# Kernel optimization log

Hardware: AMD Instinct MI355X
Metric: run time of the kernel (lower is better)

Reference implementation:

```python
import jax, jax.numpy as jnp
import numpy as np

N_NODES = 50000
NEG_SLOPE = 0.2  # PyG GATConv default
EPS = 1e-16      # PyG softmax denominator epsilon


def gat_conv(x, W, att_src, att_dst, bias, src, dst, heads, out_ch):
    # x: [N, F_in]; W: [F_in, heads*out_ch]; att_*: [heads, out_ch]
    N = x.shape[0]
    h = (x @ W).reshape(N, heads, out_ch)              # [N,H,C]
    a_src = jnp.sum(h * att_src, axis=-1)              # [N,H]
    a_dst = jnp.sum(h * att_dst, axis=-1)              # [N,H]
    alpha = a_src[src] + a_dst[dst]                    # [E,H]
    alpha = jnp.where(alpha > 0, alpha, NEG_SLOPE * alpha)  # leaky_relu
    amax = jax.ops.segment_max(alpha, dst, num_segments=N)  # [N,H]
    amax = jnp.where(jnp.isfinite(amax), amax, 0.0)
    ex = jnp.exp(alpha - amax[dst])                    # [E,H]
    denom = jax.ops.segment_sum(ex, dst, num_segments=N)    # [N,H]
    coef = ex / (denom[dst] + EPS)                     # [E,H]
    msg = h[src] * coef[:, :, None]                    # [E,H,C]
    out = jax.ops.segment_sum(msg, dst, num_segments=N)     # [N,H,C]
    return out.reshape(N, heads * out_ch) + bias


def setup_inputs() -> dict:
    key = jax.random.key(0)
    ks = jax.random.split(key, 11)
    T, N, F = 8, N_NODES, 64
    E = 1_600_000
    x = jax.random.normal(ks[0], (T, N, F), dtype=jnp.float32)
    edge_index = jax.random.randint(ks[1], (2, E), 0, N, dtype=jnp.int64)
    s = 0.1
    return {
        "x": x,
        "edge_index": edge_index,
        "W1": jax.random.normal(ks[2], (F, 64), jnp.float32) * s,
        "att_src1": jax.random.normal(ks[3], (8, 8), jnp.float32) * s,
        "att_dst1": jax.random.normal(ks[4], (8, 8), jnp.float32) * s,
        "bias1": jax.random.normal(ks[5], (64,), jnp.float32) * s,
        "W2": jax.random.normal(ks[6], (64, F), jnp.float32) * s,
        "att_src2": jax.random.normal(ks[7], (1, F), jnp.float32) * s,
        "att_dst2": jax.random.normal(ks[8], (1, F), jnp.float32) * s,
        "bias2": jax.random.normal(ks[9], (F,), jnp.float32) * s,
    }


def reference(x, edge_index, W1, att_src1, att_dst1, bias1, W2, att_src2, att_dst2, bias2):
    N = x.shape[1]
    # PyG GATConv adds self-loops by default
    loops = jnp.arange(N, dtype=edge_index.dtype)
    src = jnp.concatenate([edge_index[0], loops])
    dst = jnp.concatenate([edge_index[1], loops])

    def step(xt):  # xt: [N, F] ; dropout is identity in eval mode
        y = jax.nn.elu(gat_conv(xt, W1, att_src1, att_dst1, bias1, src, dst, 8, 8))
        y = gat_conv(y, W2, att_src2, att_dst2, bias2, src, dst, 1, xt.shape[-1])
        return jax.nn.log_softmax(y, axis=-1)

    return jax.vmap(step)(x)  # [T, N, F]
```

## Files before the change

kernel.cpp:

```cpp
#include <hip/hip_runtime.h>
#include <hip/hip_bf16.h>
#include <math.h>


typedef __hip_bfloat16 bf16;

__device__ __forceinline__ float bf2f(unsigned short u) {
    return __uint_as_float(((unsigned int)u) << 16);
}


__global__ __launch_bounds__(256) void count_edges_kernel(const int* __restrict__ dsts,
                                                          int* cnt, int E) {
    int i = blockIdx.x * 256 + threadIdx.x;
    if (i < E) atomicAdd(&cnt[dsts[i]], 1);
}

__global__ __launch_bounds__(1024) void scan_kernel(const int* __restrict__ cnt,
                                                    int* row, int* cur, int N) {
    __shared__ int ls[1024];
    int t = threadIdx.x;
    int chunk = (N + 1023) / 1024;
    int b = t * chunk;
    int sum = 0;
    for (int i = 0; i < chunk; ++i) {
        int idx = b + i;
        if (idx < N) sum += cnt[idx] + 1;
    }
    ls[t] = sum;
    __syncthreads();
    for (int off = 1; off < 1024; off <<= 1) {
        int v = (t >= off) ? ls[t - off] : 0;
        __syncthreads();
        ls[t] += v;
        __syncthreads();
    }
    int run = (t == 0) ? 0 : ls[t - 1];
    for (int i = 0; i < chunk; ++i) {
        int idx = b + i;
        if (idx < N) {
            int c = cnt[idx] + 1;
            row[idx] = run;
            cur[idx] = run;
            run += c;
        }
    }
    if (t == 1023) row[N] = ls[1023];
}

__device__ __forceinline__ void fill_csr_body(int i, const int* __restrict__ srcs,
                                              const int* __restrict__ dsts,
                                              int* cur, int* esrc, int E, int N) {
    if (i >= E + N) return;
    int s, d;
    if (i < E) { s = srcs[i]; d = dsts[i]; }
    else       { s = i - E;   d = s; }
    int pos = atomicAdd(&cur[d], 1);
    esrc[pos] = s;
}

__global__ __launch_bounds__(256) void fill_csr_kernel(const int* __restrict__ srcs,
                                                       const int* __restrict__ dsts,
                                                       int* cur, int* esrc, int E, int N) {
    fill_csr_body(blockIdx.x * 256 + threadIdx.x, srcs, dsts, cur, esrc, E, N);
}


__device__ __forceinline__ float4 ld4(const float* p) { return *(const float4*)p; }
__device__ __forceinline__ float4 ld4(const bf16* p) {
    ushort4 u = *(const ushort4*)p;
    float4 r;
    r.x = bf2f(u.x); r.y = bf2f(u.y); r.z = bf2f(u.z); r.w = bf2f(u.w);
    return r;
}


template <typename TIN, int H, int C>
__device__ __forceinline__ void gemm_att_body(
    int bid,
    const TIN* __restrict__ xin,
    const float* __restrict__ Wm,
    const float* __restrict__ att_s,
    const float* __restrict__ att_d,
    bf16* __restrict__ hout,
    float* __restrict__ asrc,
    float* __restrict__ adst,
    int R) {
    __shared__ float Ws[64 * 64];
    int tid = threadIdx.x;
    {
        const float4* W4 = (const float4*)Wm;
        float4* Ws4 = (float4*)Ws;
#pragma unroll
        for (int i = 0; i < 4; ++i) Ws4[tid + 256 * i] = W4[tid + 256 * i];
    }
    __syncthreads();

    int c  = tid & 63;
    int wv = tid >> 6;
    int n0 = (bid * 4 + wv) * 4;
    if (n0 >= R) return;
    int nrows = (R - n0 >= 4) ? 4 : (R - n0);

    const TIN* xb = xin + (size_t)n0 * 64;
    float acc[4] = {0.f, 0.f, 0.f, 0.f};

#pragma unroll 2
    for (int k4 = 0; k4 < 16; ++k4) {
        float4 xv[4];
#pragma unroll
        for (int r = 0; r < 4; ++r) {
            int rr = (r < nrows) ? r : 0;
            xv[r] = ld4(xb + (size_t)rr * 64 + k4 * 4);
        }
        float w0 = Ws[(4 * k4 + 0) * 64 + c];
        float w1 = Ws[(4 * k4 + 1) * 64 + c];
        float w2 = Ws[(4 * k4 + 2) * 64 + c];
        float w3 = Ws[(4 * k4 + 3) * 64 + c];
#pragma unroll
        for (int r = 0; r < 4; ++r) {
            acc[r] = fmaf(xv[r].x, w0, acc[r]);
            acc[r] = fmaf(xv[r].y, w1, acc[r]);
            acc[r] = fmaf(xv[r].z, w2, acc[r]);
            acc[r] = fmaf(xv[r].w, w3, acc[r]);
        }
    }

    float as_w = att_s[c];
    float ad_w = att_d[c];
#pragma unroll
    for (int r = 0; r < 4; ++r) {
        if (r >= nrows) break;
        int n = n0 + r;
        float a = acc[r];
        hout[(size_t)n * 64 + c] = __float2bfloat16(a);
        float vs = a * as_w;
        float vd = a * ad_w;
#pragma unroll
        for (int off = 1; off < C; off <<= 1) {
            vs += __shfl_xor(vs, off, 64);
            vd += __shfl_xor(vd, off, 64);
        }
        if ((c % C) == 0) {
            int hd = c / C;
            asrc[(size_t)n * H + hd] = vs;
            adst[(size_t)n * H + hd] = vd;
        }
    }
}

template <typename TIN, int H, int C>
__global__ __launch_bounds__(256) void gemm_att_kernel(
    const TIN* __restrict__ xin, const float* __restrict__ Wm,
    const float* __restrict__ att_s, const float* __restrict__ att_d,
    bf16* __restrict__ hout, float* __restrict__ asrc, float* __restrict__ adst, int R) {
    gemm_att_body<TIN, H, C>(blockIdx.x, xin, Wm, att_s, att_d, hout, asrc, adst, R);
}

template <typename TIN, int H, int C>
__global__ __launch_bounds__(256) void gemm_fill_kernel(
    const TIN* __restrict__ xin, const float* __restrict__ Wm,
    const float* __restrict__ att_s, const float* __restrict__ att_d,
    bf16* __restrict__ hout, float* __restrict__ asrc, float* __restrict__ adst, int R,
    const int* __restrict__ srcs, const int* __restrict__ dsts,
    int* cur, int* esrc, int E, int N, int fill_blocks) {
    if ((int)blockIdx.x < fill_blocks) {
        fill_csr_body((int)blockIdx.x * 256 + threadIdx.x, srcs, dsts, cur, esrc, E, N);
    } else {
        gemm_att_body<TIN, H, C>((int)blockIdx.x - fill_blocks,
                                 xin, Wm, att_s, att_d, hout, asrc, adst, R);
    }
}


template <int H, bool FINAL>
__global__ __launch_bounds__(256) void gat_edge_kernel(
    const bf16* __restrict__ h_all,
    const float* __restrict__ asrc_all,
    const float* __restrict__ adst_all,
    const int* __restrict__ row,
    const int* __restrict__ esrc,
    const float* __restrict__ bias,
    bf16* __restrict__ outb,
    float* __restrict__ outf,
    int N, int BPT) {
    int tid  = threadIdx.x;
    int lane = tid & 63;
    int t  = blockIdx.x / BPT;
    int nb = blockIdx.x - t * BPT;
    int n  = nb * 4 + (tid >> 6);
    if (n >= N) return;

    const bf16*  h     = h_all    + (size_t)t * N * 64;
    const char*  asrcb = (const char*)(asrc_all + (size_t)t * N * H);
    const float* adst  = adst_all + (size_t)t * N * H;

    const int head = (H == 8) ? (lane >> 3) : 0;
    float adn = adst[(size_t)n * H + head];

    int e0  = row[n];
    int deg = row[n + 1] - e0;

    float lsum_lane = 0.f;
    float acc0 = 0.f, acc1 = 0.f;

    for (int base = 0; base < deg; base += 64) {
        int cnt = deg - base; if (cnt > 64) cnt = 64;
        int sv = (lane < cnt) ? esrc[e0 + base + lane] : 0;

        if constexpr (H == 8) {
            unsigned head4 = (unsigned)(head << 2);
            unsigned l7_4  = (unsigned)((lane & 7) << 2);
#pragma unroll
            for (int sub = 0; sub < 8; ++sub) {
                if (sub * 8 >= cnt) break;
                int svj = __builtin_amdgcn_ds_bpermute((sub * 32) + l7_4, sv);
                unsigned aoff = (((unsigned)svj) << 5) | head4;
                float av = *(const float*)(asrcb + aoff);
                float tv = av + adn;
                tv = tv > 0.f ? tv : 0.2f * tv;
                tv = (sub * 8 + (lane & 7) < cnt) ? tv : -INFINITY;
                float p = __expf(tv);
                lsum_lane += p;
                unsigned pu = __float_as_uint(p);
#define ACC_EDGE(Q)                                                            \
    {                                                                          \
        float pj = __uint_as_float(                                            \
            __builtin_amdgcn_ds_swizzle(pu, ((Q) << 5) | 0x18));               \
        unsigned sj = (unsigned)__builtin_amdgcn_readlane(sv, sub * 8 + (Q));  \
        const unsigned short* hrow =                                           \
            (const unsigned short*)h + ((size_t)sj << 6);    \
        float hvf = bf2f(hrow[lane]);                                          \
        if ((Q) & 1) acc1 = fmaf(pj, hvf, acc1);                               \
        else         acc0 = fmaf(pj, hvf, acc0);                               \
    }
                ACC_EDGE(0) ACC_EDGE(1) ACC_EDGE(2) ACC_EDGE(3)
                ACC_EDGE(4) ACC_EDGE(5) ACC_EDGE(6) ACC_EDGE(7)
#undef ACC_EDGE
            }
        } else {
            unsigned aoff = ((unsigned)sv) << 2;
            float av = *(const float*)(asrcb + aoff);
            float tv = av + adn;
            tv = tv > 0.f ? tv : 0.2f * tv;
            tv = (lane < cnt) ? tv : -INFINITY;
            float p0 = __expf(tv);
            lsum_lane += p0;
            for (int j0 = 0; j0 < cnt; j0 += 8) {
#pragma unroll
                for (int q = 0; q < 8; ++q) {
                    int j = j0 + q;
                    float pj = __uint_as_float(
                        __builtin_amdgcn_readlane(__float_as_uint(p0), j));
                    unsigned sj = (unsigned)__builtin_amdgcn_readlane(sv, j);
                    const unsigned short* hrow =
                        (const unsigned short*)h + ((size_t)sj << 6);
                    float hvf = bf2f(hrow[lane]);
                    if (q & 1) acc1 = fmaf(pj, hvf, acc1);
                    else       acc0 = fmaf(pj, hvf, acc0);
                }
            }
        }
    }

    float lsum;
    if constexpr (H == 8) {
        float ls = lsum_lane;
        ls += __shfl_xor(ls, 1, 64);
        ls += __shfl_xor(ls, 2, 64);
        ls += __shfl_xor(ls, 4, 64);
        lsum = ls;
    } else {
        float ls = lsum_lane;
#pragma unroll
        for (int o = 1; o < 64; o <<= 1) ls += __shfl_xor(ls, o, 64);
        lsum = ls;
    }

    float v = (acc0 + acc1) / (lsum + 1e-16f) + bias[lane];
    size_t oidx = ((size_t)t * N + n) * 64 + lane;
    if (!FINAL) {
        float y = v > 0.f ? v : expm1f(v);
        outb[oidx] = __float2bfloat16(y);
    } else {
        float mx = v;
#pragma unroll
        for (int off = 1; off < 64; off <<= 1) mx = fmaxf(mx, __shfl_xor(mx, off, 64));
        float ex = __expf(v - mx);
        float sm = ex;
#pragma unroll
        for (int off = 1; off < 64; off <<= 1) sm += __shfl_xor(sm, off, 64);
        outf[oidx] = (v - mx) - __logf(sm);
    }
}


extern "C" void kernel_launch(void* const* d_in, const int* in_sizes, int n_in,
                              void* d_out, int out_size, void* d_ws, size_t ws_size,
                              hipStream_t stream) {
    const float* x        = (const float*)d_in[0];
    const int*   eidx     = (const int*)d_in[1];
    const float* W1       = (const float*)d_in[2];
    const float* att_src1 = (const float*)d_in[3];
    const float* att_dst1 = (const float*)d_in[4];
    const float* bias1    = (const float*)d_in[5];
    const float* W2       = (const float*)d_in[6];
    const float* att_src2 = (const float*)d_in[7];
    const float* att_dst2 = (const float*)d_in[8];
    const float* bias2    = (const float*)d_in[9];
    float* dout = (float*)d_out;

    const int N = 50000;
    const int F = 64;
    const int E = in_sizes[1] / 2;
    const int T = in_sizes[0] / (N * F);
    const int NT = T * N;
    const int Etot = E + N;
    const int BPT = (N + 3) / 4;

    const int* srcs = eidx;
    const int* dsts = eidx + E;

    char* ws = (char*)d_ws;
    size_t off = 0;
    auto carve = [&](size_t bytes) -> void* {
        void* p = ws + off;
        off = (off + bytes + 255) & ~(size_t)255;
        return p;
    };
    bf16*  h_all  = (bf16*)carve((size_t)NT * 64 * sizeof(bf16));
    bf16*  y1_all = (bf16*)carve((size_t)NT * 64 * sizeof(bf16));
    float* asrc   = (float*)carve((size_t)NT * 8 * sizeof(float));
    float* adst   = (float*)carve((size_t)NT * 8 * sizeof(float));
    int*   rowp   = (int*)carve((size_t)(N + 1) * sizeof(int));
    int*   cnt    = (int*)carve((size_t)N * sizeof(int));
    int*   cur    = (int*)carve((size_t)N * sizeof(int));
    int*   esrc   = (int*)carve((size_t)Etot * sizeof(int));
    bool batched = (off <= ws_size);

    if (batched) {
        hipMemsetAsync(cnt, 0, (size_t)N * sizeof(int), stream);
        count_edges_kernel<<<(E + 255) / 256, 256, 0, stream>>>(dsts, cnt, E);
        scan_kernel<<<1, 1024, 0, stream>>>(cnt, rowp, cur, N);

        int gemm_blocks = (NT + 15) / 16;
        int fill_blocks = (E + N + 255) / 256;
        int edge_grid = BPT * T;
        gemm_fill_kernel<float, 8, 8><<<fill_blocks + gemm_blocks, 256, 0, stream>>>(
            x, W1, att_src1, att_dst1, h_all, asrc, adst, NT,
            srcs, dsts, cur, esrc, E, N, fill_blocks);
        gat_edge_kernel<8, false><<<edge_grid, 256, 0, stream>>>(
            h_all, asrc, adst, rowp, esrc, bias1, y1_all, nullptr, N, BPT);
        gemm_att_kernel<bf16, 1, 64><<<gemm_blocks, 256, 0, stream>>>(
            y1_all, W2, att_src2, att_dst2, h_all, asrc, adst, NT);
        gat_edge_kernel<1, true><<<edge_grid, 256, 0, stream>>>(
            h_all, asrc, adst, rowp, esrc, bias2, nullptr, dout, N, BPT);
    } else {
        off = 0;
        bf16*  h1  = (bf16*)carve((size_t)N * 64 * sizeof(bf16));
        bf16*  y1  = (bf16*)carve((size_t)N * 64 * sizeof(bf16));
        float* as1 = (float*)carve((size_t)N * 8 * sizeof(float));
        float* ad1 = (float*)carve((size_t)N * 8 * sizeof(float));
        int*   rp  = (int*)carve((size_t)(N + 1) * sizeof(int));
        int*   cn  = (int*)carve((size_t)N * sizeof(int));
        int*   cu  = (int*)carve((size_t)N * sizeof(int));
        int*   es  = (int*)carve((size_t)Etot * sizeof(int));
        hipMemsetAsync(cn, 0, (size_t)N * sizeof(int), stream);
        count_edges_kernel<<<(E + 255) / 256, 256, 0, stream>>>(dsts, cn, E);
        scan_kernel<<<1, 1024, 0, stream>>>(cn, rp, cu, N);
        fill_csr_kernel<<<(E + N + 255) / 256, 256, 0, stream>>>(srcs, dsts, cu, es, E, N);
        int gemm_grid = (N + 15) / 16;
        for (int t = 0; t < T; ++t) {
            const float* xt = x + (size_t)t * N * F;
            float* ot = dout + (size_t)t * N * F;
            gemm_att_kernel<float, 8, 8><<<gemm_grid, 256, 0, stream>>>(
                xt, W1, att_src1, att_dst1, h1, as1, ad1, N);
            gat_edge_kernel<8, false><<<(N + 3) / 4, 256, 0, stream>>>(
                h1, as1, ad1, rp, es, bias1, y1, nullptr, N, (N + 3) / 4);
            gemm_att_kernel<bf16, 1, 64><<<gemm_grid, 256, 0, stream>>>(
                y1, W2, att_src2, att_dst2, h1, as1, ad1, N);
            gat_edge_kernel<1, true><<<(N + 3) / 4, 256, 0, stream>>>(
                h1, as1, ad1, rp, es, bias2, nullptr, ot, N, (N + 3) / 4);
        }
    }
}
```

Measured before the change: 1.164 ms.

## Batch attention gathers in edge kernel and split fused CSR-fill/GEMM launch

In the 8-head edge kernel, all eight attention-score gathers for a 64-edge chunk are now issued before any exp or accumulation, so the gather latencies overlap instead of being serialized per 8-edge sub-group. The feature gather loop then runs in 16-edge steps, and the single-head path's unroll goes from 8 to 16 to keep more loads in flight. The fused fill-CSR plus GEMM launch is split back into two separate kernels. That removes the fused launch's chance to overlap the atomic-heavy CSR fill with the GEMM, and the extra unrolling raises register pressure.

```diff
diff --git a/kernel.cpp b/kernel.cpp
--- a/kernel.cpp
+++ b/kernel.cpp
@@ -48,9 +48,10 @@
     if (t == 1023) row[N] = ls[1023];
 }
 
-__device__ __forceinline__ void fill_csr_body(int i, const int* __restrict__ srcs,
-                                              const int* __restrict__ dsts,
-                                              int* cur, int* esrc, int E, int N) {
+__global__ __launch_bounds__(256) void fill_csr_kernel(const int* __restrict__ srcs,
+                                                       const int* __restrict__ dsts,
+                                                       int* cur, int* esrc, int E, int N) {
+    int i = blockIdx.x * 256 + threadIdx.x;
     if (i >= E + N) return;
     int s, d;
     if (i < E) { s = srcs[i]; d = dsts[i]; }
@@ -59,12 +60,6 @@
     esrc[pos] = s;
 }
 
-__global__ __launch_bounds__(256) void fill_csr_kernel(const int* __restrict__ srcs,
-                                                       const int* __restrict__ dsts,
-                                                       int* cur, int* esrc, int E, int N) {
-    fill_csr_body(blockIdx.x * 256 + threadIdx.x, srcs, dsts, cur, esrc, E, N);
-}
-
 
 __device__ __forceinline__ float4 ld4(const float* p) { return *(const float4*)p; }
 __device__ __forceinline__ float4 ld4(const bf16* p) {
@@ -76,8 +71,7 @@
 
 
 template <typename TIN, int H, int C>
-__device__ __forceinline__ void gemm_att_body(
-    int bid,
+__global__ __launch_bounds__(256) void gemm_att_kernel(
     const TIN* __restrict__ xin,
     const float* __restrict__ Wm,
     const float* __restrict__ att_s,
@@ -98,7 +92,7 @@
 
     int c  = tid & 63;
     int wv = tid >> 6;
-    int n0 = (bid * 4 + wv) * 4;
+    int n0 = (blockIdx.x * 4 + wv) * 4;
     if (n0 >= R) return;
     int nrows = (R - n0 >= 4) ? 4 : (R - n0);
 
@@ -146,29 +140,6 @@
             asrc[(size_t)n * H + hd] = vs;
             adst[(size_t)n * H + hd] = vd;
         }
-    }
-}
-
-template <typename TIN, int H, int C>
-__global__ __launch_bounds__(256) void gemm_att_kernel(
-    const TIN* __restrict__ xin, const float* __restrict__ Wm,
-    const float* __restrict__ att_s, const float* __restrict__ att_d,
-    bf16* __restrict__ hout, float* __restrict__ asrc, float* __restrict__ adst, int R) {
-    gemm_att_body<TIN, H, C>(blockIdx.x, xin, Wm, att_s, att_d, hout, asrc, adst, R);
-}
-
-template <typename TIN, int H, int C>
-__global__ __launch_bounds__(256) void gemm_fill_kernel(
-    const TIN* __restrict__ xin, const float* __restrict__ Wm,
-    const float* __restrict__ att_s, const float* __restrict__ att_d,
-    bf16* __restrict__ hout, float* __restrict__ asrc, float* __restrict__ adst, int R,
-    const int* __restrict__ srcs, const int* __restrict__ dsts,
-    int* cur, int* esrc, int E, int N, int fill_blocks) {
-    if ((int)blockIdx.x < fill_blocks) {
-        fill_csr_body((int)blockIdx.x * 256 + threadIdx.x, srcs, dsts, cur, esrc, E, N);
-    } else {
-        gemm_att_body<TIN, H, C>((int)blockIdx.x - fill_blocks,
-                                 xin, Wm, att_s, att_d, hout, asrc, adst, R);
     }
 }
 
@@ -211,33 +182,47 @@
         if constexpr (H == 8) {
             unsigned head4 = (unsigned)(head << 2);
             unsigned l7_4  = (unsigned)((lane & 7) << 2);
+            float av[8];
 #pragma unroll
             for (int sub = 0; sub < 8; ++sub) {
-                if (sub * 8 >= cnt) break;
-                int svj = __builtin_amdgcn_ds_bpermute((sub * 32) + l7_4, sv);
-                unsigned aoff = (((unsigned)svj) << 5) | head4;
-                float av = *(const float*)(asrcb + aoff);
-                float tv = av + adn;
+                int svj = __builtin_amdgcn_ds_bpermute(sub * 32 + l7_4, sv);
+                av[sub] = *(const float*)(asrcb + ((((unsigned)svj) << 5) | head4));
+            }
+            float p[8];
+#pragma unroll
+            for (int sub = 0; sub < 8; ++sub) {
+                float tv = av[sub] + adn;
                 tv = tv > 0.f ? tv : 0.2f * tv;
                 tv = (sub * 8 + (lane & 7) < cnt) ? tv : -INFINITY;
-                float p = __expf(tv);
-                lsum_lane += p;
-                unsigned pu = __float_as_uint(p);
-#define ACC_EDGE(Q)                                                            \
+                p[sub] = __expf(tv);
+                lsum_lane += p[sub];
+            }
+#define ACC_EDGE(SUB, Q)                                                       \
     {                                                                          \
-        float pj = __uint_as_float(                                            \
-            __builtin_amdgcn_ds_swizzle(pu, ((Q) << 5) | 0x18));               \
-        unsigned sj = (unsigned)__builtin_amdgcn_readlane(sv, sub * 8 + (Q));  \
+        float pj = __uint_as_float(__builtin_amdgcn_ds_swizzle(                \
+            __float_as_uint(p[(SUB)]), ((Q) << 5) | 0x18));                    \
+        unsigned sj = (unsigned)__builtin_amdgcn_readlane(sv, (SUB) * 8 + (Q));\
         const unsigned short* hrow =                                           \
             (const unsigned short*)h + ((size_t)sj << 6);    \
         float hvf = bf2f(hrow[lane]);                                          \
         if ((Q) & 1) acc1 = fmaf(pj, hvf, acc1);                               \
         else         acc0 = fmaf(pj, hvf, acc0);                               \
     }
-                ACC_EDGE(0) ACC_EDGE(1) ACC_EDGE(2) ACC_EDGE(3)
-                ACC_EDGE(4) ACC_EDGE(5) ACC_EDGE(6) ACC_EDGE(7)
+#define ACC_SUB(SUB)                                                           \
+    ACC_EDGE(SUB, 0) ACC_EDGE(SUB, 1) ACC_EDGE(SUB, 2) ACC_EDGE(SUB, 3)        \
+    ACC_EDGE(SUB, 4) ACC_EDGE(SUB, 5) ACC_EDGE(SUB, 6) ACC_EDGE(SUB, 7)
+#pragma unroll
+            for (int s2 = 0; s2 < 4; ++s2) {
+                if (s2 * 16 >= cnt) break;
+                switch (s2) {
+                    case 0: ACC_SUB(0) ACC_SUB(1) break;
+                    case 1: ACC_SUB(2) ACC_SUB(3) break;
+                    case 2: ACC_SUB(4) ACC_SUB(5) break;
+                    default: ACC_SUB(6) ACC_SUB(7) break;
+                }
+            }
+#undef ACC_SUB
 #undef ACC_EDGE
-            }
         } else {
             unsigned aoff = ((unsigned)sv) << 2;
             float av = *(const float*)(asrcb + aoff);
@@ -246,9 +231,9 @@
             tv = (lane < cnt) ? tv : -INFINITY;
             float p0 = __expf(tv);
             lsum_lane += p0;
-            for (int j0 = 0; j0 < cnt; j0 += 8) {
-#pragma unroll
-                for (int q = 0; q < 8; ++q) {
+            for (int j0 = 0; j0 < cnt; j0 += 16) {
+#pragma unroll
+                for (int q = 0; q < 16; ++q) {
                     int j = j0 + q;
                     float pj = __uint_as_float(
                         __builtin_amdgcn_readlane(__float_as_uint(p0), j));
@@ -342,13 +327,12 @@
         hipMemsetAsync(cnt, 0, (size_t)N * sizeof(int), stream);
         count_edges_kernel<<<(E + 255) / 256, 256, 0, stream>>>(dsts, cnt, E);
         scan_kernel<<<1, 1024, 0, stream>>>(cnt, rowp, cur, N);
+        fill_csr_kernel<<<(E + N + 255) / 256, 256, 0, stream>>>(srcs, dsts, cur, esrc, E, N);
 
         int gemm_blocks = (NT + 15) / 16;
-        int fill_blocks = (E + N + 255) / 256;
         int edge_grid = BPT * T;
-        gemm_fill_kernel<float, 8, 8><<<fill_blocks + gemm_blocks, 256, 0, stream>>>(
-            x, W1, att_src1, att_dst1, h_all, asrc, adst, NT,
-            srcs, dsts, cur, esrc, E, N, fill_blocks);
+        gemm_att_kernel<float, 8, 8><<<gemm_blocks, 256, 0, stream>>>(
+            x, W1, att_src1, att_dst1, h_all, asrc, adst, NT);
         gat_edge_kernel<8, false><<<edge_grid, 256, 0, stream>>>(
             h_all, asrc, adst, rowp, esrc, bias1, y1_all, nullptr, N, BPT);
         gemm_att_kernel<bf16, 1, 64><<<gemm_blocks, 256, 0, stream>>>(
```

New measurement: 1.264 ms. 1.09x slower.
